# Optimization experiments

Hardware: AMD Instinct MI355X
Metric: run time of the kernel (lower is better)

Reference implementation:

```python
import jax, jax.numpy as jnp
import numpy as np

B, T, D, H = 4, 2048, 1024, 16
HD = D // H


def setup_inputs() -> dict:
    key = jax.random.key(0)
    ks = jax.random.split(key, 10)
    s = 1.0 / np.sqrt(D)
    # xavier_uniform bound for wbias [T,T]: sqrt(6/(T+T))
    wb_bound = float(np.sqrt(6.0 / (T + T)))
    return {
        "x": jax.random.normal(ks[0], (B, T, D), dtype=jnp.float32),
        "Wq": jax.random.normal(ks[1], (D, D), dtype=jnp.float32) * s,
        "bq": jnp.zeros((D,), dtype=jnp.float32),
        "Wk": jax.random.normal(ks[2], (D, D), dtype=jnp.float32) * s,
        "bk": jnp.zeros((D,), dtype=jnp.float32),
        "Wv": jax.random.normal(ks[3], (D, D), dtype=jnp.float32) * s,
        "bv": jnp.zeros((D,), dtype=jnp.float32),
        "Wo": jax.random.normal(ks[4], (D, D), dtype=jnp.float32) * s,
        "bo": jnp.zeros((D,), dtype=jnp.float32),
        "wbias": jax.random.uniform(ks[5], (T, T), dtype=jnp.float32,
                                    minval=-wb_bound, maxval=wb_bound),
    }


def reference(x, Wq, bq, Wk, bk, Wv, bv, Wo, bo, wbias):
    Bc, Tc, Dc = x.shape
    # projections, split heads: [B, H, T, HD]
    def proj(W, b):
        y = x @ W + b
        return y.reshape(Bc, Tc, H, HD).transpose(0, 2, 1, 3)

    Q = proj(Wq, bq)
    K = proj(Wk, bk)
    V = proj(Wv, bv)

    Q_sig = jax.nn.sigmoid(Q)
    eK = jnp.exp(K)                      # [B,H,T,HD]
    ew = jnp.exp(wbias[:Tc, :Tc])        # [T,T]

    num = jnp.einsum('ts,bhsd->bhtd', ew, eK * V)
    den = jnp.einsum('ts,bhsd->bhtd', ew, eK)
    out = Q_sig * (num / den)            # [B,H,T,HD]

    out = out.transpose(0, 2, 1, 3).reshape(Bc, Tc, Dc)
    return out @ Wo + bo
```

## Files before the change

kernel.cpp:

```cpp
#include <hip/hip_runtime.h>
#include <hip/hip_bf16.h>


#define AS1(p) ((const __attribute__((address_space(1))) void*)(p))
#define AS3(p) ((__attribute__((address_space(3))) void*)(p))

typedef _Float16 half8 __attribute__((ext_vector_type(8)));
typedef _Float16 half4v __attribute__((ext_vector_type(4)));
typedef float floatx16 __attribute__((ext_vector_type(16)));

__device__ __forceinline__ long frag_off(int r, int k) {
  return (long)(((((r >> 5) * 4 + (k >> 4)) * 2 + ((k >> 3) & 1)) * 32 + (r & 31)) * 8 + (k & 7));
}


__global__ __launch_bounds__(256) void prep_all(
    const float* __restrict__ x, const float* __restrict__ wb, const float* __restrict__ Wq,
    const float* __restrict__ Wk, const float* __restrict__ Wv, const float* __restrict__ Wo,
    _Float16* __restrict__ x_h, _Float16* __restrict__ ew_h, _Float16* __restrict__ WqkvT,
    _Float16* __restrict__ WoT) {
  __shared__ _Float16 lds[64 * 132];
  const int bid = blockIdx.x;
  const int tid = threadIdx.x;

  if (bid < 1536) {
    const bool isx = bid < 1024;
    const float* src;
    _Float16* dst;
    int tm, tk, ld, trel;
    if (isx) {
      trel = bid; tm = bid >> 4; tk = bid & 15; src = x; dst = x_h; ld = 1024;
    } else {
      trel = bid - 1024; tm = trel >> 5; tk = trel & 31; src = wb; dst = ew_h; ld = 2048;
    }
    const long tbase = (long)trel * 8192;
#pragma unroll
    for (int p = 0; p < 4; ++p) {
      const int s = p * 256 + tid;
      const int r = ((s >> 8) << 5) + (s & 31);
      const int k = ((s >> 6) & 3) * 16 + ((s >> 5) & 1) * 8;
      const float* sp = src + (long)(tm * 128 + r) * ld + tk * 64 + k;
      const float4 v0 = *(const float4*)sp;
      const float4 v1 = *(const float4*)(sp + 4);
      half8 h;
      if (isx) {
        h[0] = (_Float16)v0.x; h[1] = (_Float16)v0.y; h[2] = (_Float16)v0.z; h[3] = (_Float16)v0.w;
        h[4] = (_Float16)v1.x; h[5] = (_Float16)v1.y; h[6] = (_Float16)v1.z; h[7] = (_Float16)v1.w;
      } else {
        h[0] = (_Float16)__expf(v0.x); h[1] = (_Float16)__expf(v0.y);
        h[2] = (_Float16)__expf(v0.z); h[3] = (_Float16)__expf(v0.w);
        h[4] = (_Float16)__expf(v1.x); h[5] = (_Float16)__expf(v1.y);
        h[6] = (_Float16)__expf(v1.z); h[7] = (_Float16)__expf(v1.w);
      }
      *(half8*)(dst + tbase + (long)s * 8) = h;
    }
    return;
  }

  const int b2 = bid - 1536;
  const float* src0;
  const float* src1 = nullptr;
  _Float16* dst;
  int tn, tk, cb = 0;
  if (b2 < 128) {
    tn = b2 >> 4; tk = b2 & 15; src0 = Wq; dst = WqkvT;
  } else if (b2 < 384) {
    const int t = b2 - 128;
    tn = 8 + (t >> 4); tk = t & 15; cb = (tn - 8) * 64; src0 = Wk; src1 = Wv; dst = WqkvT;
  } else {
    const int t = b2 - 384;
    tn = t >> 4; tk = t & 15; src0 = Wo; dst = WoT;
  }
  if (!src1) {
#pragma unroll
    for (int p = 0; p < 8; ++p) {
      const int kl = p * 8 + (tid >> 5);
      const int cl = (tid & 31) * 4;
      const float4 v = *(const float4*)(src0 + (long)(tk * 64 + kl) * 1024 + tn * 128 + cl);
      half4v h;
      h[0] = (_Float16)v.x; h[1] = (_Float16)v.y; h[2] = (_Float16)v.z; h[3] = (_Float16)v.w;
      *(half4v*)(lds + kl * 132 + cl) = h;
    }
  } else {
#pragma unroll
    for (int m = 0; m < 2; ++m) {
      const float* s = m ? src1 : src0;
      const int rb = m ? 32 : 0;
#pragma unroll
      for (int p = 0; p < 4; ++p) {
        const int kl = p * 16 + (tid >> 4);
        const int cl = (tid & 15) * 4;
        const int rl = (cl >> 5) * 64 + rb + (cl & 31);
        const float4 v = *(const float4*)(s + (long)(tk * 64 + kl) * 1024 + cb + cl);
        half4v h;
        h[0] = (_Float16)v.x; h[1] = (_Float16)v.y; h[2] = (_Float16)v.z; h[3] = (_Float16)v.w;
        *(half4v*)(lds + kl * 132 + rl) = h;
      }
    }
  }
  __syncthreads();
  const long tbase = (long)(tn * 16 + tk) * 8192;
#pragma unroll
  for (int p = 0; p < 4; ++p) {
    const int s = p * 256 + tid;
    const int r = ((s >> 8) << 5) + (s & 31);
    const int kl = ((s >> 6) & 3) * 16 + ((s >> 5) & 1) * 8;
    half8 h;
#pragma unroll
    for (int j = 0; j < 8; ++j) h[j] = lds[(kl + j) * 132 + r];
    *(half8*)(dst + tbase + (long)s * 8) = h;
  }
}

template <int MODE>
__global__ __launch_bounds__(256) void gemm_bt(
    const _Float16* __restrict__ A, const _Float16* __restrict__ Bt, void* __restrict__ Cv,
    int Ktiles, long batchB, const float* __restrict__ bias0, const float* __restrict__ bias1,
    const float* __restrict__ bias2, const _Float16* __restrict__ Qsig,
    _Float16* __restrict__ Zt) {
  __shared__ __align__(16) _Float16 sA[8192];
  __shared__ __align__(16) _Float16 sB[8192];
  const int tid = threadIdx.x;
  const int wave = tid >> 6, lane = tid & 63;
  const int l32 = lane & 31, khalf = lane >> 5;

  const int gx = gridDim.x, gy = gridDim.y;
  const int tot = gx * gy * gridDim.z;
  const int f = blockIdx.x + gx * (blockIdx.y + gy * blockIdx.z);
  const int nid = (f & 7) * (tot >> 3) + (f >> 3);
  const int bxs = nid % gx;
  const int bys = (nid / gx) % gy;
  const int bzs = nid / (gx * gy);

  const int m0 = bxs * 128, n0 = bys * 128;
  const int wm = (wave >> 1) * 64, wn = (wave & 1) * 64;

  const _Float16* Atile = A + (long)bxs * Ktiles * 8192;
  const _Float16* Btile = Bt + (long)bzs * batchB + (long)bys * Ktiles * 8192;

  floatx16 acc[2][2] = {};

  for (int tk = 0; tk < Ktiles; ++tk) {
    const _Float16* As = Atile + tk * 8192 + wave * 512 + lane * 8;
    const _Float16* Bs = Btile + tk * 8192 + wave * 512 + lane * 8;
#pragma unroll
    for (int c = 0; c < 4; ++c) {
      __builtin_amdgcn_global_load_lds(AS1(As + c * 2048), AS3(sA + c * 2048 + wave * 512), 16, 0, 0);
      __builtin_amdgcn_global_load_lds(AS1(Bs + c * 2048), AS3(sB + c * 2048 + wave * 512), 16, 0, 0);
    }
    __syncthreads();
#pragma unroll
    for (int ks = 0; ks < 4; ++ks) {
      half8 af[2], bf[2];
#pragma unroll
      for (int i = 0; i < 2; ++i) {
        af[i] = *(const half8*)(sA + (((wm >> 5) + i) * 4 + ks) * 512 + lane * 8);
        bf[i] = *(const half8*)(sB + (((wn >> 5) + i) * 4 + ks) * 512 + lane * 8);
      }
#pragma unroll
      for (int mt = 0; mt < 2; ++mt)
#pragma unroll
        for (int nt = 0; nt < 2; ++nt)
          acc[mt][nt] =
              __builtin_amdgcn_mfma_f32_32x32x16_f16(af[mt], bf[nt], acc[mt][nt], 0, 0, 0);
    }
    __syncthreads();
  }

  if (MODE == 0) {
    if (n0 < 1024) {
      _Float16* Qs = (_Float16*)Cv;
#pragma unroll
      for (int mt = 0; mt < 2; ++mt) {
        const long ttile = (m0 + wm + mt * 32) >> 5;
#pragma unroll
        for (int nt = 0; nt < 2; ++nt) {
          const int col = n0 + wn + nt * 32 + l32;
          const float bb = bias0[col];
          const long base = (ttile * 32 + (((n0 + wn) >> 5) + nt)) * 1024;
#pragma unroll
          for (int q = 0; q < 4; ++q) {
            half4v o;
#pragma unroll
            for (int rr = 0; rr < 4; ++rr) {
              const float v = acc[mt][nt][q * 4 + rr] + bb;
              o[rr] = (_Float16)(1.0f / (1.0f + __expf(-v)));
            }
            *(half4v*)(Qs + base + q * 256 + lane * 4) = o;
          }
        }
      }
    } else {
      const int g = (n0 - 1024 + wn) >> 6;
      const int ch = g * 32 + l32;
      const float bkc = bias1[ch], bvc = bias2[ch];
      const int jn = g * 64 + l32;
      const long tnbase = (long)(jn >> 7) * 32 * 8192;
#pragma unroll
      for (int mt = 0; mt < 2; ++mt) {
#pragma unroll
        for (int q = 0; q < 4; ++q) {
          half4v numv, denv;
#pragma unroll
          for (int rr = 0; rr < 4; ++rr) {
            const float ek = __expf(acc[mt][0][q * 4 + rr] + bkc);
            const float vv = acc[mt][1][q * 4 + rr] + bvc;
            denv[rr] = (_Float16)ek;
            numv[rr] = (_Float16)(ek * vv);
          }
          const int row = m0 + wm + mt * 32 + 4 * khalf + 8 * q;
          const int b = row >> 11, s = row & 2047;
          const long off = (long)b * 4194304 + tnbase + (long)(s >> 6) * 8192 +
                           frag_off(jn & 127, s & 63);
          *(half4v*)(Zt + off) = numv;
          *(half4v*)(Zt + off + 2048) = denv;
        }
      }
    }
    return;
  }

  if (MODE == 3) {
    const int ch = ((n0 + wn) >> 6) * 32 + l32;
    _Float16* OH = (_Float16*)Cv;
#pragma unroll
    for (int mt = 0; mt < 2; ++mt) {
      const long ttile = (long)(bzs * 2048 + m0 + wm + mt * 32) >> 5;
      const long qbase = (ttile * 32 + ((n0 + wn) >> 6)) * 1024;
#pragma unroll
      for (int q = 0; q < 4; ++q) {
        const half4v qv = *(const half4v*)(Qsig + qbase + q * 256 + lane * 4);
#pragma unroll
        for (int rr = 0; rr < 4; ++rr) {
          const int reg = q * 4 + rr;
          const float num = acc[mt][0][reg], den = acc[mt][1][reg];
          const int r = m0 + wm + mt * 32 + 4 * khalf + 8 * q + rr;
          const int R = bzs * 2048 + r;
          const long off = ((long)(R >> 7) * 16 + (ch >> 6)) * 8192 + frag_off(R & 127, ch & 63);
          OH[off] = (_Float16)((float)qv[rr] * num / den);
        }
      }
    }
    return;
  }

#pragma unroll
  for (int mt = 0; mt < 2; ++mt)
#pragma unroll
    for (int nt = 0; nt < 2; ++nt) {
      const int col = n0 + wn + nt * 32 + l32;
      const float bb = bias0[col];
#pragma unroll
      for (int reg = 0; reg < 16; ++reg) {
        const int row = m0 + wm + mt * 32 + 4 * khalf + 8 * (reg >> 2) + (reg & 3);
        ((float*)Cv)[(long)row * 1024 + col] = acc[mt][nt][reg] + bb;
      }
    }
}

extern "C" void kernel_launch(void* const* d_in, const int* in_sizes, int n_in, void* d_out,
                              int out_size, void* d_ws, size_t ws_size, hipStream_t stream) {
  const float* x = (const float*)d_in[0];
  const float* Wq = (const float*)d_in[1];
  const float* bq = (const float*)d_in[2];
  const float* Wk = (const float*)d_in[3];
  const float* bk = (const float*)d_in[4];
  const float* Wv = (const float*)d_in[5];
  const float* bv = (const float*)d_in[6];
  const float* Wo = (const float*)d_in[7];
  const float* bo = (const float*)d_in[8];
  const float* wb = (const float*)d_in[9];

  char* ws = (char*)d_ws;
  _Float16* x_h = (_Float16*)(ws + 0);
  _Float16* WqkvT = (_Float16*)(ws + 16777216);
  _Float16* WoT = (_Float16*)(ws + 23068672);
  _Float16* ew_h = (_Float16*)(ws + 25165824);
  _Float16* Qsig = (_Float16*)(ws + 33554432);
  _Float16* Zt = (_Float16*)(ws + 50331648);
  _Float16* OutHead = (_Float16*)(ws + 83886080);

  prep_all<<<2048, 256, 0, stream>>>(x, wb, Wq, Wk, Wv, Wo, x_h, ew_h, WqkvT, WoT);

  gemm_bt<0><<<dim3(64, 24, 1), 256, 0, stream>>>(x_h, WqkvT, Qsig, 16, 0, bq, bk, bv, nullptr,
                                                  Zt);

  gemm_bt<3><<<dim3(16, 16, 4), 256, 0, stream>>>(ew_h, Zt, OutHead, 32, (long)4194304, nullptr,
                                                  nullptr, nullptr, Qsig, nullptr);

  gemm_bt<2><<<dim3(64, 8, 1), 256, 0, stream>>>(OutHead, WoT, d_out, 16, 0, bo, nullptr,
                                                 nullptr, nullptr, nullptr);
}
```

Baseline: 293.9 us.

## Run the exp-weight attention GEMM in FP8 with exp(w)-1 decomposition

Measured after the change: 272.9 us. 7.1% less time.

```diff
diff --git a/kernel.cpp b/kernel.cpp
--- a/kernel.cpp
+++ b/kernel.cpp
@@ -8,56 +8,64 @@
 typedef _Float16 half8 __attribute__((ext_vector_type(8)));
 typedef _Float16 half4v __attribute__((ext_vector_type(4)));
 typedef float floatx16 __attribute__((ext_vector_type(16)));
+typedef int intx4 __attribute__((ext_vector_type(4)));
+typedef int intx8 __attribute__((ext_vector_type(8)));
 
 __device__ __forceinline__ long frag_off(int r, int k) {
   return (long)(((((r >> 5) * 4 + (k >> 4)) * 2 + ((k >> 3) & 1)) * 32 + (r & 31)) * 8 + (k & 7));
 }
-
+__device__ __forceinline__ long off8(int r, int k) {
+  return (long)((((((r >> 5) * 2 + ((k >> 6) & 1)) * 2 + ((k >> 4) & 1)) * 2 + ((k >> 5) & 1)) * 32 +
+                 (r & 31)) * 16 + (k & 15));
+}
 
 __global__ __launch_bounds__(256) void prep_all(
     const float* __restrict__ x, const float* __restrict__ wb, const float* __restrict__ Wq,
     const float* __restrict__ Wk, const float* __restrict__ Wv, const float* __restrict__ Wo,
-    _Float16* __restrict__ x_h, _Float16* __restrict__ ew_h, _Float16* __restrict__ WqkvT,
+    _Float16* __restrict__ x_h, char* __restrict__ E8, _Float16* __restrict__ WqkvT,
     _Float16* __restrict__ WoT) {
   __shared__ _Float16 lds[64 * 132];
   const int bid = blockIdx.x;
   const int tid = threadIdx.x;
 
-  if (bid < 1536) {
-    const bool isx = bid < 1024;
-    const float* src;
-    _Float16* dst;
-    int tm, tk, ld, trel;
-    if (isx) {
-      trel = bid; tm = bid >> 4; tk = bid & 15; src = x; dst = x_h; ld = 1024;
-    } else {
-      trel = bid - 1024; tm = trel >> 5; tk = trel & 31; src = wb; dst = ew_h; ld = 2048;
-    }
-    const long tbase = (long)trel * 8192;
+  if (bid < 1024) {
+    const int tm = bid >> 4, tk = bid & 15;
+    const long tbase = (long)bid * 8192;
 #pragma unroll
     for (int p = 0; p < 4; ++p) {
       const int s = p * 256 + tid;
       const int r = ((s >> 8) << 5) + (s & 31);
       const int k = ((s >> 6) & 3) * 16 + ((s >> 5) & 1) * 8;
-      const float* sp = src + (long)(tm * 128 + r) * ld + tk * 64 + k;
+      const float* sp = x + (long)(tm * 128 + r) * 1024 + tk * 64 + k;
       const float4 v0 = *(const float4*)sp;
       const float4 v1 = *(const float4*)(sp + 4);
       half8 h;
-      if (isx) {
-        h[0] = (_Float16)v0.x; h[1] = (_Float16)v0.y; h[2] = (_Float16)v0.z; h[3] = (_Float16)v0.w;
-        h[4] = (_Float16)v1.x; h[5] = (_Float16)v1.y; h[6] = (_Float16)v1.z; h[7] = (_Float16)v1.w;
-      } else {
-        h[0] = (_Float16)__expf(v0.x); h[1] = (_Float16)__expf(v0.y);
-        h[2] = (_Float16)__expf(v0.z); h[3] = (_Float16)__expf(v0.w);
-        h[4] = (_Float16)__expf(v1.x); h[5] = (_Float16)__expf(v1.y);
-        h[6] = (_Float16)__expf(v1.z); h[7] = (_Float16)__expf(v1.w);
-      }
-      *(half8*)(dst + tbase + (long)s * 8) = h;
+      h[0] = (_Float16)v0.x; h[1] = (_Float16)v0.y; h[2] = (_Float16)v0.z; h[3] = (_Float16)v0.w;
+      h[4] = (_Float16)v1.x; h[5] = (_Float16)v1.y; h[6] = (_Float16)v1.z; h[7] = (_Float16)v1.w;
+      *(half8*)(x_h + tbase + (long)s * 8) = h;
     }
     return;
   }
 
-  const int b2 = bid - 1536;
+  if (bid >= 1536) {
+    const int e = bid - 1536;
+    const int tt = e >> 4, ts = e & 15;
+    char* dst = E8 + (long)e * 16384;
+#pragma unroll
+    for (int p = 0; p < 16; ++p) {
+      const int idx = p * 256 + tid;
+      const int r = idx >> 5, k = (idx & 31) * 4;
+      const float4 v = *(const float4*)(wb + (long)(tt * 128 + r) * 2048 + ts * 128 + k);
+      const float e0 = (__expf(v.x) - 1.0f) * 32.0f, e1 = (__expf(v.y) - 1.0f) * 32.0f;
+      const float e2 = (__expf(v.z) - 1.0f) * 32.0f, e3 = (__expf(v.w) - 1.0f) * 32.0f;
+      int pk = __builtin_amdgcn_cvt_pk_fp8_f32(e0, e1, 0, false);
+      pk = __builtin_amdgcn_cvt_pk_fp8_f32(e2, e3, pk, true);
+      *(int*)(dst + off8(r, k)) = pk;
+    }
+    return;
+  }
+
+  const int b2 = bid - 1024;
   const float* src0;
   const float* src1 = nullptr;
   _Float16* dst;
@@ -115,28 +123,25 @@
 template <int MODE>
 __global__ __launch_bounds__(256) void gemm_bt(
     const _Float16* __restrict__ A, const _Float16* __restrict__ Bt, void* __restrict__ Cv,
-    int Ktiles, long batchB, const float* __restrict__ bias0, const float* __restrict__ bias1,
-    const float* __restrict__ bias2, const _Float16* __restrict__ Qsig,
-    _Float16* __restrict__ Zt) {
+    int Ktiles, const float* __restrict__ bias0, const float* __restrict__ bias1,
+    const float* __restrict__ bias2, char* __restrict__ Zt8, float* __restrict__ cs) {
   __shared__ __align__(16) _Float16 sA[8192];
   __shared__ __align__(16) _Float16 sB[8192];
   const int tid = threadIdx.x;
   const int wave = tid >> 6, lane = tid & 63;
   const int l32 = lane & 31, khalf = lane >> 5;
 
-  const int gx = gridDim.x, gy = gridDim.y;
-  const int tot = gx * gy * gridDim.z;
-  const int f = blockIdx.x + gx * (blockIdx.y + gy * blockIdx.z);
+  const int gx = gridDim.x;
+  const int tot = gx * gridDim.y;
+  const int f = blockIdx.x + gx * blockIdx.y;
   const int nid = (f & 7) * (tot >> 3) + (f >> 3);
-  const int bxs = nid % gx;
-  const int bys = (nid / gx) % gy;
-  const int bzs = nid / (gx * gy);
+  const int bxs = nid % gx, bys = nid / gx;
 
   const int m0 = bxs * 128, n0 = bys * 128;
   const int wm = (wave >> 1) * 64, wn = (wave & 1) * 64;
 
   const _Float16* Atile = A + (long)bxs * Ktiles * 8192;
-  const _Float16* Btile = Bt + (long)bzs * batchB + (long)bys * Ktiles * 8192;
+  const _Float16* Btile = Bt + (long)bys * Ktiles * 8192;
 
   floatx16 acc[2][2] = {};
 
@@ -195,51 +200,36 @@
       const int ch = g * 32 + l32;
       const float bkc = bias1[ch], bvc = bias2[ch];
       const int jn = g * 64 + l32;
-      const long tnbase = (long)(jn >> 7) * 32 * 8192;
+      const int b = m0 >> 11;
+      char* Z8 = Zt8 + (long)b * 4194304 +
+                 ((long)(jn >> 7) * 16 + ((m0 & 2047) >> 7)) * 16384;
+      const int jnl = jn & 127;
+      float sk = 0.f, sz = 0.f;
 #pragma unroll
       for (int mt = 0; mt < 2; ++mt) {
 #pragma unroll
         for (int q = 0; q < 4; ++q) {
-          half4v numv, denv;
+          float ekv[4], ekk[4];
 #pragma unroll
           for (int rr = 0; rr < 4; ++rr) {
             const float ek = __expf(acc[mt][0][q * 4 + rr] + bkc);
             const float vv = acc[mt][1][q * 4 + rr] + bvc;
-            denv[rr] = (_Float16)ek;
-            numv[rr] = (_Float16)(ek * vv);
+            ekk[rr] = ek;
+            ekv[rr] = ek * vv;
+            sk += ek;
+            sz += ek * vv;
           }
-          const int row = m0 + wm + mt * 32 + 4 * khalf + 8 * q;
-          const int b = row >> 11, s = row & 2047;
-          const long off = (long)b * 4194304 + tnbase + (long)(s >> 6) * 8192 +
-                           frag_off(jn & 127, s & 63);
-          *(half4v*)(Zt + off) = numv;
-          *(half4v*)(Zt + off + 2048) = denv;
+          const int sl = wm + mt * 32 + 4 * khalf + 8 * q;
+          int pn = __builtin_amdgcn_cvt_pk_fp8_f32(ekv[0] * 0.25f, ekv[1] * 0.25f, 0, false);
+          pn = __builtin_amdgcn_cvt_pk_fp8_f32(ekv[2] * 0.25f, ekv[3] * 0.25f, pn, true);
+          int pd = __builtin_amdgcn_cvt_pk_fp8_f32(ekk[0] * 0.25f, ekk[1] * 0.25f, 0, false);
+          pd = __builtin_amdgcn_cvt_pk_fp8_f32(ekk[2] * 0.25f, ekk[3] * 0.25f, pd, true);
+          *(int*)(Z8 + off8(jnl, sl)) = pn;
+          *(int*)(Z8 + off8(jnl + 32, sl)) = pd;
         }
       }
-    }
-    return;
-  }
-
-  if (MODE == 3) {
-    const int ch = ((n0 + wn) >> 6) * 32 + l32;
-    _Float16* OH = (_Float16*)Cv;
-#pragma unroll
-    for (int mt = 0; mt < 2; ++mt) {
-      const long ttile = (long)(bzs * 2048 + m0 + wm + mt * 32) >> 5;
-      const long qbase = (ttile * 32 + ((n0 + wn) >> 6)) * 1024;
-#pragma unroll
-      for (int q = 0; q < 4; ++q) {
-        const half4v qv = *(const half4v*)(Qsig + qbase + q * 256 + lane * 4);
-#pragma unroll
-        for (int rr = 0; rr < 4; ++rr) {
-          const int reg = q * 4 + rr;
-          const float num = acc[mt][0][reg], den = acc[mt][1][reg];
-          const int r = m0 + wm + mt * 32 + 4 * khalf + 8 * q + rr;
-          const int R = bzs * 2048 + r;
-          const long off = ((long)(R >> 7) * 16 + (ch >> 6)) * 8192 + frag_off(R & 127, ch & 63);
-          OH[off] = (_Float16)((float)qv[rr] * num / den);
-        }
-      }
+      atomicAdd(&cs[(long)b * 2048 + ch * 2], sz);
+      atomicAdd(&cs[(long)b * 2048 + ch * 2 + 1], sk);
     }
     return;
   }
@@ -256,6 +246,83 @@
         ((float*)Cv)[(long)row * 1024 + col] = acc[mt][nt][reg] + bb;
       }
     }
+}
+
+__global__ __launch_bounds__(256) void gemm2_fp8(
+    const char* __restrict__ E8, const char* __restrict__ Zt8, _Float16* __restrict__ OH,
+    const _Float16* __restrict__ Qsig, const float* __restrict__ cs) {
+  __shared__ __align__(16) char sA[16384];
+  __shared__ __align__(16) char sB[16384];
+  const int tid = threadIdx.x;
+  const int wave = tid >> 6, lane = tid & 63;
+  const int l32 = lane & 31, khalf = lane >> 5;
+
+  const int f = blockIdx.x + 16 * (blockIdx.y + 16 * blockIdx.z);
+  const int nid = (f & 7) * 128 + (f >> 3);
+  const int bxs = nid & 15, bys = (nid >> 4) & 15, bzs = nid >> 8;
+
+  const int m0 = bxs * 128, n0 = bys * 128;
+  const int wm = (wave >> 1) * 64, wn = (wave & 1) * 64;
+
+  const char* At = E8 + (long)bxs * 16 * 16384;
+  const char* Bt = Zt8 + (long)bzs * 4194304 + (long)bys * 16 * 16384;
+
+  floatx16 acc[2][2] = {};
+
+  for (int tk = 0; tk < 16; ++tk) {
+    const char* As = At + tk * 16384 + wave * 1024 + lane * 16;
+    const char* Bs = Bt + tk * 16384 + wave * 1024 + lane * 16;
+#pragma unroll
+    for (int c = 0; c < 4; ++c) {
+      __builtin_amdgcn_global_load_lds(AS1(As + c * 4096), AS3(sA + c * 4096 + wave * 1024), 16, 0, 0);
+      __builtin_amdgcn_global_load_lds(AS1(Bs + c * 4096), AS3(sB + c * 4096 + wave * 1024), 16, 0, 0);
+    }
+    __syncthreads();
+#pragma unroll
+    for (int ks = 0; ks < 2; ++ks) {
+      intx8 a8[2], b8[2];
+#pragma unroll
+      for (int i = 0; i < 2; ++i) {
+        const char* pa = sA + (((wm >> 5) + i) * 2 + ks) * 2048 + khalf * 512 + l32 * 16;
+        const intx4 alo = *(const intx4*)pa;
+        const intx4 ahi = *(const intx4*)(pa + 1024);
+        a8[i] = __builtin_shufflevector(alo, ahi, 0, 1, 2, 3, 4, 5, 6, 7);
+        const char* pb = sB + (((wn >> 5) + i) * 2 + ks) * 2048 + khalf * 512 + l32 * 16;
+        const intx4 blo = *(const intx4*)pb;
+        const intx4 bhi = *(const intx4*)(pb + 1024);
+        b8[i] = __builtin_shufflevector(blo, bhi, 0, 1, 2, 3, 4, 5, 6, 7);
+      }
+#pragma unroll
+      for (int mt = 0; mt < 2; ++mt)
+#pragma unroll
+        for (int nt = 0; nt < 2; ++nt)
+          acc[mt][nt] = __builtin_amdgcn_mfma_scale_f32_32x32x64_f8f6f4(
+              a8[mt], b8[nt], acc[mt][nt], 0, 0, 0, 127u, 0, 127u);
+    }
+    __syncthreads();
+  }
+
+  const int ch = ((n0 + wn) >> 6) * 32 + l32;
+  const float2 c2 = *(const float2*)(cs + (long)bzs * 2048 + ch * 2);
+#pragma unroll
+  for (int mt = 0; mt < 2; ++mt) {
+    const long ttile = (long)(bzs * 2048 + m0 + wm + mt * 32) >> 5;
+    const long qbase = (ttile * 32 + ((n0 + wn) >> 6)) * 1024;
+#pragma unroll
+    for (int q = 0; q < 4; ++q) {
+      const half4v qv = *(const half4v*)(Qsig + qbase + q * 256 + lane * 4);
+#pragma unroll
+      for (int rr = 0; rr < 4; ++rr) {
+        const int reg = q * 4 + rr;
+        const float num = c2.x + acc[mt][0][reg] * 0.125f;
+        const float den = c2.y + acc[mt][1][reg] * 0.125f;
+        const int r = m0 + wm + mt * 32 + 4 * khalf + 8 * q + rr;
+        const int R = bzs * 2048 + r;
+        const long off = ((long)(R >> 7) * 16 + (ch >> 6)) * 8192 + frag_off(R & 127, ch & 63);
+        OH[off] = (_Float16)((float)qv[rr] * num / den);
+      }
+    }
+  }
 }
 
 extern "C" void kernel_launch(void* const* d_in, const int* in_sizes, int n_in, void* d_out,
@@ -275,19 +342,20 @@
   _Float16* x_h = (_Float16*)(ws + 0);
   _Float16* WqkvT = (_Float16*)(ws + 16777216);
   _Float16* WoT = (_Float16*)(ws + 23068672);
-  _Float16* ew_h = (_Float16*)(ws + 25165824);
-  _Float16* Qsig = (_Float16*)(ws + 33554432);
-  _Float16* Zt = (_Float16*)(ws + 50331648);
-  _Float16* OutHead = (_Float16*)(ws + 83886080);
-
-  prep_all<<<2048, 256, 0, stream>>>(x, wb, Wq, Wk, Wv, Wo, x_h, ew_h, WqkvT, WoT);
-
-  gemm_bt<0><<<dim3(64, 24, 1), 256, 0, stream>>>(x_h, WqkvT, Qsig, 16, 0, bq, bk, bv, nullptr,
-                                                  Zt);
-
-  gemm_bt<3><<<dim3(16, 16, 4), 256, 0, stream>>>(ew_h, Zt, OutHead, 32, (long)4194304, nullptr,
-                                                  nullptr, nullptr, Qsig, nullptr);
-
-  gemm_bt<2><<<dim3(64, 8, 1), 256, 0, stream>>>(OutHead, WoT, d_out, 16, 0, bo, nullptr,
-                                                 nullptr, nullptr, nullptr);
-}
+  char* E8 = (char*)(ws + 25165824);
+  _Float16* Qsig = (_Float16*)(ws + 29360128);
+  char* Zt8 = (char*)(ws + 46137344);
+  _Float16* OutHead = (_Float16*)(ws + 62914560);
+  float* cs = (float*)(ws + 79691776);
+
+  hipMemsetAsync(cs, 0, 4 * 2048 * sizeof(float), stream);
+
+  prep_all<<<1792, 256, 0, stream>>>(x, wb, Wq, Wk, Wv, Wo, x_h, E8, WqkvT, WoT);
+
+  gemm_bt<0><<<dim3(64, 24), 256, 0, stream>>>(x_h, WqkvT, Qsig, 16, bq, bk, bv, Zt8, cs);
+
+  gemm2_fp8<<<dim3(16, 16, 4), 256, 0, stream>>>(E8, Zt8, OutHead, Qsig, cs);
+
+  gemm_bt<2><<<dim3(64, 8), 256, 0, stream>>>(OutHead, WoT, d_out, 16, bo, nullptr, nullptr,
+                                              nullptr, nullptr);
+}
```
